# Performance work log

Measured on AMD Instinct MI355X. Metric: run time of the kernel, lower is better.

Reference implementation:

```python
import jax, jax.numpy as jnp
import numpy as np

M = 4  # mixture size of the AttentionStem value embedding

def unfold_windows(a, kh, kw, Hout, Wout):
    # a: [..., Hp, Wp] -> [..., Hout, Wout, kh, kw] (stride-1 sliding windows, cropped)
    rows = []
    for i in range(kh):
        cols = [a[..., i:i + Hout, j:j + Wout] for j in range(kw)]
        rows.append(jnp.stack(cols, axis=-1))
    return jnp.stack(rows, axis=-2)

def attention_stem(x, qw, kw_, vw, emb_a, emb_b, emb_mix, kh, kw, pad):
    # x: [B,Cin,H,W]; qw/kw_: [Cin,Co]; vw: [M,Cin,Co]; emb_a:[Co,kh]; emb_b:[Co,kw]; emb_mix:[M,Co]
    B, Cin, H, W = x.shape
    pl, pr, pt, pb = pad  # F.pad order (left,right,top,bottom)
    xp = jnp.pad(x, ((0, 0), (0, 0), (pt, pb), (pl, pr)))
    Hp, Wp = xp.shape[2], xp.shape[3]
    Hout = min(Hp - kh + 1, H)
    Wout = min(Wp - kw + 1, W)
    q = jnp.einsum('bchw,co->bohw', x[:, :, :Hout, :Wout], qw)       # 1x1 conv query
    k = jnp.einsum('bchw,co->bohw', xp, kw_)                          # 1x1 conv key on padded
    v = jnp.einsum('bchw,mco->mbohw', xp, vw)                         # m 1x1 conv values
    k_win = unfold_windows(k, kh, kw, Hout, Wout)                     # [B,Co,Ho,Wo,kh,kw]
    v_win = unfold_windows(v, kh, kw, Hout, Wout)                     # [M,B,Co,Ho,Wo,kh,kw]
    # mixture relative-position embedding, softmax over mixtures per (kh,kw) offset
    la = emb_mix @ emb_a                                              # [M,kh]
    lb = emb_mix @ emb_b                                              # [M,kw]
    emb = jax.nn.softmax(la[:, :, None] + lb[:, None, :], axis=0)     # [M,kh,kw]
    v_agg = jnp.einsum('mkl,mbohwkl->bohwkl', emb, v_win)             # [B,Co,Ho,Wo,kh,kw]
    K = kh * kw
    scores = jnp.einsum('bohw,bohwkl->bhwkl', q, k_win).reshape(B, Hout, Wout, K)
    attn = jax.nn.softmax(scores, axis=-1).reshape(B, Hout, Wout, kh, kw)
    out = jnp.einsum('bhwkl,bohwkl->bohw', attn, v_agg)               # [B,Co,Ho,Wo]
    return out

def bn_relu(x, g, b):
    # training-mode BatchNorm2d + ReLU
    mu = x.mean(axis=(0, 2, 3), keepdims=True)
    var = x.var(axis=(0, 2, 3), keepdims=True)
    y = (x - mu) * jax.lax.rsqrt(var + 1e-5) * g[None, :, None, None] + b[None, :, None, None]
    return jax.nn.relu(y)

def _params(key):
    ks = jax.random.split(key, 18)
    def w(k, shape):
        return jax.random.normal(k, shape, dtype=jnp.float32) * 0.1
    cfg = [(1, 64, 1, 5), (64, 128, 2, 5), (128, 16, 2, 5)]
    p = {}
    i = 0
    for s, (ci, co, kh, kw) in enumerate(cfg):
        p[f'p{s}_q'] = w(ks[i], (ci, co)); i += 1
        p[f'p{s}_k'] = w(ks[i], (ci, co)); i += 1
        p[f'p{s}_v'] = w(ks[i], (M, ci, co)); i += 1
        p[f'p{s}_ea'] = w(ks[i], (co, kh)); i += 1
        p[f'p{s}_eb'] = w(ks[i], (co, kw)); i += 1
        p[f'p{s}_em'] = w(ks[i], (M, co)); i += 1
        p[f'p{s}_g'] = jnp.ones((co,), jnp.float32)
        p[f'p{s}_b'] = jnp.zeros((co,), jnp.float32)
    return p

def setup_inputs() -> dict:
    key = jax.random.key(0)
    kx, kp = jax.random.split(key)
    inp = {'x': jax.random.normal(kx, (2, 1, 8, 3000), dtype=jnp.float32)}
    inp.update(_params(kp))
    return inp

def reference(x,
              p0_q, p0_k, p0_v, p0_ea, p0_eb, p0_em, p0_g, p0_b,
              p1_q, p1_k, p1_v, p1_ea, p1_eb, p1_em, p1_g, p1_b,
              p2_q, p2_k, p2_v, p2_ea, p2_eb, p2_em, p2_g, p2_b):
    h = attention_stem(x, p0_q, p0_k, p0_v, p0_ea, p0_eb, p0_em, 1, 5, (2, 2, 0, 0))
    h = bn_relu(h, p0_g, p0_b)[:, :, ::2, ::2]                        # MaxPool2d(1,2) == stride-2 subsample
    h = attention_stem(h, p1_q, p1_k, p1_v, p1_ea, p1_eb, p1_em, 2, 5, (2, 2, 1, 1))
    h = bn_relu(h, p1_g, p1_b)[:, :, ::2, ::2]
    h = attention_stem(h, p2_q, p2_k, p2_v, p2_ea, p2_eb, p2_em, 2, 5, (2, 2, 0, 0))
    h = bn_relu(h, p2_g, p2_b)
    B, C, H, W = h.shape
    nW = W // 56                                                       # AvgPool2d((1,56))
    return h[:, :, :, :nW * 56].reshape(B, C, H, nW, 56).mean(-1)
```

## Files before the change

### kernel.cpp

```cpp
#include <hip/hip_runtime.h>
#include <math.h>


#define TPB 256

__global__ void prep0_kernel(const float* __restrict__ ea,
                             const float* __restrict__ eb,
                             const float* __restrict__ em,
                             const float* __restrict__ qw,
                             const float* __restrict__ kw_,
                             const float* __restrict__ vw,
                             float* __restrict__ par) {
    const int M4 = 4, Co = 64, kh = 1, kw = 5;
    __shared__ float la[4];
    __shared__ float lb[20];
    __shared__ float embs[20];
    int tid = threadIdx.x;
    if (tid < 64) {
        float p = qw[tid] * kw_[tid];
#pragma unroll
        for (int d = 1; d < 64; d <<= 1) p += __shfl_xor(p, d, 64);
        if (tid == 0) par[0] = p;
    }
    if (tid >= 64 && tid < 64 + M4) {
        int m = tid - 64;
        float s = 0.f;
        for (int o = 0; o < Co; ++o) s += em[m * Co + o] * ea[o];
        la[m] = s;
    }
    if (tid >= 128 && tid < 128 + M4 * kw) {
        int r = tid - 128;
        int m = r / kw, l = r % kw;
        float s = 0.f;
        for (int o = 0; o < Co; ++o) s += em[m * Co + o] * eb[o * kw + l];
        lb[m * kw + l] = s;
    }
    __syncthreads();
    if (tid < 5) {
        float lg[4];
        float mx = -1e30f;
        for (int m = 0; m < M4; ++m) {
            lg[m] = la[m] + lb[m * kw + tid];
            mx = fmaxf(mx, lg[m]);
        }
        float sum = 0.f;
        for (int m = 0; m < M4; ++m) { lg[m] = expf(lg[m] - mx); sum += lg[m]; }
        float inv = 1.f / sum;
        for (int m = 0; m < M4; ++m) embs[tid * 4 + m] = lg[m] * inv;
    }
    __syncthreads();
    for (int e = tid; e < 5 * 64; e += blockDim.x) {
        int t = e / 64, o = e - t * 64;
        float s = 0.f;
        for (int m = 0; m < M4; ++m) s += embs[t * 4 + m] * vw[m * 64 + o];
        par[1 + e] = s;
    }
}

__global__ void prep_wcat_kernel(const float* __restrict__ ea,
                                 const float* __restrict__ eb,
                                 const float* __restrict__ em,
                                 const float* __restrict__ qw,
                                 const float* __restrict__ kw_,
                                 const float* __restrict__ vw,
                                 float* __restrict__ Wcat,
                                 int Co, int kh, int kw, int Cin) {
    const int M4 = 4;
    __shared__ float la[8];
    __shared__ float lb[20];
    __shared__ float embs[40];
    int K = kh * kw;
    int tid = threadIdx.x;
    if (tid < M4 * kh) {
        int m = tid / kh, k = tid % kh;
        float s = 0.f;
        for (int o = 0; o < Co; ++o) s += em[m * Co + o] * ea[o * kh + k];
        la[tid] = s;
    }
    if (tid >= 64 && tid < 64 + M4 * kw) {
        int r = tid - 64;
        int m = r / kw, l = r % kw;
        float s = 0.f;
        for (int o = 0; o < Co; ++o) s += em[m * Co + o] * eb[o * kw + l];
        lb[r] = s;
    }
    __syncthreads();
    if (tid < K) {
        int k = tid / kw, l = tid % kw;
        float lg[4];
        float mx = -1e30f;
        for (int m = 0; m < M4; ++m) {
            lg[m] = la[m * kh + k] + lb[m * kw + l];
            mx = fmaxf(mx, lg[m]);
        }
        float sum = 0.f;
        for (int m = 0; m < M4; ++m) { lg[m] = expf(lg[m] - mx); sum += lg[m]; }
        float inv = 1.f / sum;
        for (int m = 0; m < M4; ++m) embs[tid * 4 + m] = lg[m] * inv;
    }
    __syncthreads();
    int Mtot = (2 + K) * Co;
    long long total = (long long)Mtot * Cin;
    for (long long e = (long long)blockIdx.x * blockDim.x + tid; e < total;
         e += (long long)gridDim.x * blockDim.x) {
        int m = (int)(e / Cin);
        int c = (int)(e - (long long)m * Cin);
        float val;
        if (m < Co) {
            val = qw[c * Co + m];
        } else if (m < 2 * Co) {
            val = kw_[c * Co + (m - Co)];
        } else {
            int mz = m - 2 * Co;
            int t = mz / Co;
            int o = mz - t * Co;
            val = 0.f;
            for (int mm = 0; mm < M4; ++mm)
                val += embs[t * 4 + mm] * vw[(mm * Cin + c) * Co + o];
        }
        Wcat[e] = val;
    }
}

__global__ void attn_out0_kernel(const float* __restrict__ x,
                                 const float* __restrict__ par,
                                 float* __restrict__ s0) {
    __shared__ float wsh[5][256];
    __shared__ float vsh[5 * 64];
    int tid = threadIdx.x;
    int b = blockIdx.y;
    int n0 = blockIdx.x * 256;
    int n = n0 + tid;
    for (int i = tid; i < 320; i += 256) vsh[i] = par[1 + i];
    float c0 = par[0];
    if (n < 24000) {
        int h = n / 3000, w = n - h * 3000;
        const float* xr = x + b * 24000 + h * 3000;
        float xc = xr[w];
        float xs[5], s[5];
#pragma unroll
        for (int t = 0; t < 5; ++t) {
            int col = w + t - 2;
            xs[t] = (col >= 0 && col < 3000) ? xr[col] : 0.f;
            s[t] = c0 * xc * xs[t];
        }
        float mx = s[0];
#pragma unroll
        for (int t = 1; t < 5; ++t) mx = fmaxf(mx, s[t]);
        float sum = 0.f;
#pragma unroll
        for (int t = 0; t < 5; ++t) { s[t] = expf(s[t] - mx); sum += s[t]; }
        float inv = 1.f / sum;
#pragma unroll
        for (int t = 0; t < 5; ++t) wsh[t][tid] = s[t] * inv * xs[t];
    } else {
#pragma unroll
        for (int t = 0; t < 5; ++t) wsh[t][tid] = 0.f;
    }
    __syncthreads();
    int jq = tid & 63, og = tid >> 6;
    int nq = n0 + jq * 4;
    if (nq < 24000) {
        float wq[5][4];
#pragma unroll
        for (int t = 0; t < 5; ++t)
#pragma unroll
            for (int j = 0; j < 4; ++j) wq[t][j] = wsh[t][jq * 4 + j];
        int obase = og * 16;
        for (int oi = 0; oi < 16; ++oi) {
            int o = obase + oi;
            float4 v;
            v.x = 0.f; v.y = 0.f; v.z = 0.f; v.w = 0.f;
#pragma unroll
            for (int t = 0; t < 5; ++t) {
                float vo = vsh[t * 64 + o];
                v.x = fmaf(wq[t][0], vo, v.x);
                v.y = fmaf(wq[t][1], vo, v.y);
                v.z = fmaf(wq[t][2], vo, v.z);
                v.w = fmaf(wq[t][3], vo, v.w);
            }
            *(float4*)&s0[((size_t)b * 64 + o) * 24000 + nq] = v;
        }
    }
}

__launch_bounds__(256, 2)
__global__ void gemm_qkz_kernel(const float* __restrict__ A,
                                const float* __restrict__ X,
                                float* __restrict__ qk,
                                float* __restrict__ z,
                                int M, int N, int K, int twoCo) {
    __shared__ float As[64][132];
    __shared__ float Bs[64][132];
    int tid = threadIdx.x;
    int b = blockIdx.z;
    int m0 = blockIdx.y * 128, n0 = blockIdx.x * 128;
    int Mz = M - twoCo;
    float acc[8][8] = {{0.f}};
    int am = tid >> 1, ak = (tid & 1) * 32;
    int bk = tid >> 2, bn = (tid & 3) * 32;
    int tm = tid & 15, tn = tid >> 4;

    for (int k0 = 0; k0 < K; k0 += 64) {
        {
            int mA = m0 + am;
            const float* Ap = A + (size_t)mA * K + k0 + ak;
#pragma unroll
            for (int q = 0; q < 8; ++q) {
                float4 v = (mA < M) ? *(const float4*)(Ap + q * 4)
                                    : make_float4(0.f, 0.f, 0.f, 0.f);
                int kk = ak + q * 4;
                As[kk + 0][am] = v.x;
                As[kk + 1][am] = v.y;
                As[kk + 2][am] = v.z;
                As[kk + 3][am] = v.w;
            }
        }
        {
            const float* Xp = X + (size_t)b * K * N + (size_t)(k0 + bk) * N + n0 + bn;
            if (n0 + 128 <= N) {
#pragma unroll
                for (int q = 0; q < 8; ++q)
                    *(float4*)&Bs[bk][bn + q * 4] = *(const float4*)(Xp + q * 4);
            } else {
#pragma unroll
                for (int q = 0; q < 8; ++q)
#pragma unroll
                    for (int j = 0; j < 4; ++j) {
                        int n = n0 + bn + q * 4 + j;
                        Bs[bk][bn + q * 4 + j] = (n < N) ? Xp[q * 4 + j] : 0.f;
                    }
            }
        }
        __syncthreads();
#pragma unroll 16
        for (int k = 0; k < 64; ++k) {
            float4 a0 = *(const float4*)&As[k][tm * 8];
            float4 a1 = *(const float4*)&As[k][tm * 8 + 4];
            float4 b0 = *(const float4*)&Bs[k][tn * 8];
            float4 b1 = *(const float4*)&Bs[k][tn * 8 + 4];
            float av[8] = {a0.x, a0.y, a0.z, a0.w, a1.x, a1.y, a1.z, a1.w};
            float bv[8] = {b0.x, b0.y, b0.z, b0.w, b1.x, b1.y, b1.z, b1.w};
#pragma unroll
            for (int i = 0; i < 8; ++i)
#pragma unroll
                for (int j = 0; j < 8; ++j)
                    acc[i][j] = fmaf(av[i], bv[j], acc[i][j]);
        }
        __syncthreads();
    }
    bool fullN = (n0 + 128 <= N);
#pragma unroll
    for (int i = 0; i < 8; ++i) {
        int m = m0 + tm * 8 + i;
        if (m >= M) continue;
        if (m < twoCo) {
#pragma unroll
            for (int j = 0; j < 8; ++j) {
                int n = n0 + tn * 8 + j;
                if (n < N) qk[((size_t)b * N + n) * twoCo + m] = acc[i][j];
            }
        } else {
            float* zp = &z[((size_t)b * Mz + (m - twoCo)) * N + n0 + tn * 8];
            if (fullN) {
                *(float4*)zp = make_float4(acc[i][0], acc[i][1], acc[i][2], acc[i][3]);
                *(float4*)(zp + 4) = make_float4(acc[i][4], acc[i][5], acc[i][6], acc[i][7]);
            } else {
#pragma unroll
                for (int j = 0; j < 8; ++j) {
                    int n = n0 + tn * 8 + j;
                    if (n < N) zp[j] = acc[i][j];
                }
            }
        }
    }
}

template <int KH, int KW, int CO, int NPB>
__global__ void attn_v3_kernel(const float* __restrict__ qk,
                               float* __restrict__ attn,
                               int H, int W, int Ho, int Wo, int pt, int pl) {
    const int K = KH * KW;
    __shared__ float ssh[NPB][K];
    int tid = threadIdx.x;
    int b = blockIdx.y;
    int ln = tid / K, t = tid - ln * K;
    int Nout = Ho * Wo;
    int n = blockIdx.x * NPB + ln;
    bool active = (tid < NPB * K) && (n < Nout);
    int HWin = H * W;
    float sv = 0.f;
    int ho = 0, wo = 0;
    if (active) {
        ho = n / Wo; wo = n - ho * Wo;
        int row = ho + t / KW - pt, col = wo + t % KW - pl;
        if (row >= 0 && row < H && col >= 0 && col < W) {
            const float* qp = qk + ((size_t)b * HWin + ho * W + wo) * (2 * CO);
            const float* kp = qk + ((size_t)b * HWin + (size_t)row * W + col) * (2 * CO) + CO;
#pragma unroll
            for (int o = 0; o < CO; o += 4) {
                float4 q4 = *(const float4*)(qp + o);
                float4 k4 = *(const float4*)(kp + o);
                sv += q4.x * k4.x + q4.y * k4.y + q4.z * k4.z + q4.w * k4.w;
            }
        }
        ssh[ln][t] = sv;
    }
    __syncthreads();
    if (active) {
        float mx = ssh[ln][0];
#pragma unroll
        for (int tt = 1; tt < K; ++tt) mx = fmaxf(mx, ssh[ln][tt]);
        float sum = 0.f;
#pragma unroll
        for (int tt = 0; tt < K; ++tt) sum += expf(ssh[ln][tt] - mx);
        float num = expf(sv - mx);
        attn[((size_t)b * K + t) * Nout + n] = num / sum;
    }
}

template <int KH, int KW>
__global__ void combine_kernel(const float* __restrict__ z,
                               const float* __restrict__ attn,
                               float* __restrict__ out,
                               int B, int Co, int Mz,
                               int H, int W, int Ho, int Wo,
                               int pt, int pl) {
    const int K = KH * KW;
    int idx = blockIdx.x * blockDim.x + threadIdx.x;
    int N = B * Co * Ho * Wo;
    if (idx >= N) return;
    int wo = idx % Wo; int r = idx / Wo;
    int ho = r % Ho; r /= Ho;
    int o = r % Co; int b = r / Co;
    int Nin = H * W, Nout = Ho * Wo;
    int nout = ho * Wo + wo;
    float acc = 0.f;
#pragma unroll
    for (int dk = 0; dk < KH; ++dk) {
        int row = ho + dk - pt;
        if (row < 0 || row >= H) continue;
#pragma unroll
        for (int dl = 0; dl < KW; ++dl) {
            int col = wo + dl - pl;
            if (col < 0 || col >= W) continue;
            int t = dk * KW + dl;
            float a = attn[((size_t)b * K + t) * Nout + nout];
            float zv = z[((size_t)b * Mz + t * Co + o) * Nin + row * W + col];
            acc = fmaf(a, zv, acc);
        }
    }
    out[idx] = acc;
}

__global__ void bn_partial_kernel(const float* __restrict__ x,
                                  float2* __restrict__ part,
                                  int B, int C, int HW, int len) {
    int c = blockIdx.x, ch = blockIdx.y, NCH = gridDim.y;
    int tid = threadIdx.x;
    int start = ch * len;
    int end = min(HW, start + len);
    float s = 0.f, s2 = 0.f;
    bool vec = ((HW & 3) == 0) && ((len & 3) == 0);
    for (int b = 0; b < B; ++b) {
        const float* xp = x + ((size_t)b * C + c) * HW;
        if (vec) {
            for (int i = start + tid * 4; i < end; i += TPB * 4) {
                float4 v = *(const float4*)(xp + i);
                s += v.x + v.y + v.z + v.w;
                s2 += v.x * v.x + v.y * v.y + v.z * v.z + v.w * v.w;
            }
        } else {
            for (int i = start + tid; i < end; i += TPB) {
                float v = xp[i];
                s += v; s2 += v * v;
            }
        }
    }
    __shared__ float sh[TPB], sh2[TPB];
    sh[tid] = s; sh2[tid] = s2;
    __syncthreads();
    for (int st = TPB / 2; st > 0; st >>= 1) {
        if (tid < st) { sh[tid] += sh[tid + st]; sh2[tid] += sh2[tid + st]; }
        __syncthreads();
    }
    if (tid == 0) part[c * NCH + ch] = make_float2(sh[0], sh2[0]);
}

__global__ void bn_final_kernel(const float2* __restrict__ part,
                                float* __restrict__ mr,
                                int C, int NCH, int B, int HW) {
    int c = threadIdx.x;
    if (c >= C) return;
    double s = 0.0, s2 = 0.0;
    for (int i = 0; i < NCH; ++i) {
        float2 p = part[c * NCH + i];
        s += p.x; s2 += p.y;
    }
    double N = (double)B * HW;
    double mean = s / N;
    double var = s2 / N - mean * mean;
    mr[c] = (float)mean;
    mr[C + c] = (float)(1.0 / sqrt(var + 1e-5));
}

__global__ void bn_pool_kernel(const float* __restrict__ x,
                               const float* __restrict__ mr,
                               const float* __restrict__ g,
                               const float* __restrict__ bb,
                               float* __restrict__ y,
                               int B, int C, int H, int W, int H2, int W2) {
    int idx = blockIdx.x * blockDim.x + threadIdx.x;
    int N = B * C * H2 * W2;
    if (idx >= N) return;
    int w2 = idx % W2; int r = idx / W2;
    int h2 = r % H2; r /= H2;
    int c = r % C; int b = r / C;
    float v = x[(((long long)b * C + c) * H + 2 * h2) * W + 2 * w2];
    float yn = (v - mr[c]) * mr[C + c] * g[c] + bb[c];
    y[idx] = fmaxf(yn, 0.f);
}

__global__ void bn_avg_final_kernel(const float* __restrict__ x,
                                    const float* __restrict__ mr,
                                    const float* __restrict__ g,
                                    const float* __restrict__ bb,
                                    float* __restrict__ out,
                                    int B, int C, int W, int nW) {
    int idx = blockIdx.x * blockDim.x + threadIdx.x;
    int N = B * C * nW;
    if (idx >= N) return;
    int j = idx % nW; int r = idx / nW;
    int c = r % C; int b = r / C;
    float mean = mr[c], rstd = mr[C + c], gg = g[c], bo = bb[c];
    const float* xb = x + ((long long)b * C + c) * W + j * 56;
    float s = 0.f;
    for (int i = 0; i < 56; ++i) {
        float yn = (xb[i] - mean) * rstd * gg + bo;
        s += fmaxf(yn, 0.f);
    }
    out[idx] = s * (1.f / 56.f);
}

extern "C" void kernel_launch(void* const* d_in, const int* in_sizes, int n_in,
                              void* d_out, int out_size, void* d_ws, size_t ws_size,
                              hipStream_t stream) {
    const float* x   = (const float*)d_in[0];
    const float* qw0 = (const float*)d_in[1];
    const float* kw0 = (const float*)d_in[2];
    const float* vw0 = (const float*)d_in[3];
    const float* ea0 = (const float*)d_in[4];
    const float* eb0 = (const float*)d_in[5];
    const float* em0 = (const float*)d_in[6];
    const float* g0  = (const float*)d_in[7];
    const float* b0  = (const float*)d_in[8];
    const float* qw1 = (const float*)d_in[9];
    const float* kw1 = (const float*)d_in[10];
    const float* vw1 = (const float*)d_in[11];
    const float* ea1 = (const float*)d_in[12];
    const float* eb1 = (const float*)d_in[13];
    const float* em1 = (const float*)d_in[14];
    const float* g1  = (const float*)d_in[15];
    const float* b1  = (const float*)d_in[16];
    const float* qw2 = (const float*)d_in[17];
    const float* kw2 = (const float*)d_in[18];
    const float* vw2 = (const float*)d_in[19];
    const float* ea2 = (const float*)d_in[20];
    const float* eb2 = (const float*)d_in[21];
    const float* em2 = (const float*)d_in[22];
    const float* g2  = (const float*)d_in[23];
    const float* b2  = (const float*)d_in[24];
    float* outp = (float*)d_out;
    (void)ws_size; (void)in_sizes; (void)n_in; (void)out_size;

    float* ws = (float*)d_ws;
    size_t off = 0;
    auto alloc = [&](size_t n) { float* p = ws + off; off += (n + 63) & ~(size_t)63; return p; };

    float* arena = alloc(2 * 1280 * 6000);
    float* s0    = arena;
    float* z1    = arena;

    float* par0   = alloc(321);
    float* part   = alloc(2048);
    float* mr0    = alloc(2 * 64);
    float* h0     = alloc(2 * 64 * 6000);
    float* Wcat1  = alloc(1536 * 64);
    float* qk1    = alloc(2 * 6000 * 256);
    float* attn1  = alloc(2 * 10 * 6000);
    float* s1     = alloc(2 * 128 * 6000);
    float* mr1    = alloc(2 * 128);
    float* h1     = alloc(2 * 128 * 1500);
    float* Wcat2  = alloc(192 * 128);
    float* qk2    = alloc(2 * 1500 * 32);
    float* z2     = alloc(2 * 160 * 1500);
    float* attn2  = alloc(2 * 10 * 750);
    float* s2     = alloc(2 * 16 * 750);
    float* mr2    = alloc(2 * 16);

    auto grid = [](int n) { return (n + TPB - 1) / TPB; };

    prep0_kernel<<<1, TPB, 0, stream>>>(ea0, eb0, em0, qw0, kw0, vw0, par0);
    {
        dim3 g(94, 2);
        attn_out0_kernel<<<g, TPB, 0, stream>>>(x, par0, s0);
    }
    {
        dim3 g(64, 8);
        bn_partial_kernel<<<g, TPB, 0, stream>>>(s0, (float2*)part, 2, 64, 24000, 3000);
    }
    bn_final_kernel<<<1, 64, 0, stream>>>((const float2*)part, mr0, 64, 8, 2, 24000);
    bn_pool_kernel<<<grid(2 * 64 * 6000), TPB, 0, stream>>>(s0, mr0, g0, b0, h0,
        2, 64, 8, 3000, 4, 1500);

    prep_wcat_kernel<<<96, TPB, 0, stream>>>(ea1, eb1, em1, qw1, kw1, vw1, Wcat1,
        128, 2, 5, 64);
    {
        dim3 g((6000 + 127) / 128, 1536 / 128, 2);
        gemm_qkz_kernel<<<g, TPB, 0, stream>>>(Wcat1, h0, qk1, z1, 1536, 6000, 64, 256);
    }
    {
        dim3 g(6000 / 25, 2);
        attn_v3_kernel<2, 5, 128, 25><<<g, TPB, 0, stream>>>(qk1, attn1,
            4, 1500, 4, 1500, 1, 2);
    }
    combine_kernel<2, 5><<<grid(2 * 128 * 6000), TPB, 0, stream>>>(z1, attn1, s1,
        2, 128, 1280, 4, 1500, 4, 1500, 1, 2);
    {
        dim3 g(128, 4);
        bn_partial_kernel<<<g, TPB, 0, stream>>>(s1, (float2*)part, 2, 128, 6000, 1500);
    }
    bn_final_kernel<<<1, 128, 0, stream>>>((const float2*)part, mr1, 128, 4, 2, 6000);
    bn_pool_kernel<<<grid(2 * 128 * 1500), TPB, 0, stream>>>(s1, mr1, g1, b1, h1,
        2, 128, 4, 1500, 2, 750);

    prep_wcat_kernel<<<24, TPB, 0, stream>>>(ea2, eb2, em2, qw2, kw2, vw2, Wcat2,
        16, 2, 5, 128);
    {
        dim3 g((1500 + 127) / 128, (192 + 127) / 128, 2);
        gemm_qkz_kernel<<<g, TPB, 0, stream>>>(Wcat2, h1, qk2, z2, 192, 1500, 128, 32);
    }
    {
        dim3 g(750 / 25, 2);
        attn_v3_kernel<2, 5, 16, 25><<<g, TPB, 0, stream>>>(qk2, attn2,
            2, 750, 1, 750, 0, 2);
    }
    combine_kernel<2, 5><<<grid(2 * 16 * 750), TPB, 0, stream>>>(z2, attn2, s2,
        2, 16, 160, 2, 750, 1, 750, 0, 2);
    {
        dim3 g(16, 4);
        bn_partial_kernel<<<g, TPB, 0, stream>>>(s2, (float2*)part, 2, 16, 750, 188);
    }
    bn_final_kernel<<<1, 16, 0, stream>>>((const float2*)part, mr2, 16, 4, 2, 750);
    bn_avg_final_kernel<<<grid(2 * 16 * 13), TPB, 0, stream>>>(s2, mr2, g2, b2, outp,
        2, 16, 750, 13);
}
```

Baseline: 287.8 us.

## Fuse BatchNorm statistics into producer kernels and retile the QKZ GEMM

BatchNorm partial sums are now computed inside the kernels that produce each stage's output (attn_out0 and a new combine_stats kernel). The final mean/rstd reduction is folded into prep_wcat or bn_avg_final, which removes six separate bn_partial/bn_final launches and one extra pass over each activation tensor. The GEMM tile uses a K-step of 32 with a strided thread-to-output mapping and launch bounds of 4 blocks per CU, aiming for higher occupancy and vectorised qk stores. The cost is some redundant per-thread reductions in the final kernel and more warp shuffles in the first stage.

```diff
diff --git a/kernel.cpp b/kernel.cpp
--- a/kernel.cpp
+++ b/kernel.cpp
@@ -11,7 +11,7 @@
                              const float* __restrict__ kw_,
                              const float* __restrict__ vw,
                              float* __restrict__ par) {
-    const int M4 = 4, Co = 64, kh = 1, kw = 5;
+    const int M4 = 4, Co = 64, kw = 5;
     __shared__ float la[4];
     __shared__ float lb[20];
     __shared__ float embs[20];
@@ -64,13 +64,27 @@
                                  const float* __restrict__ kw_,
                                  const float* __restrict__ vw,
                                  float* __restrict__ Wcat,
-                                 int Co, int kh, int kw, int Cin) {
+                                 int Co, int kh, int kw, int Cin,
+                                 const float2* __restrict__ part,
+                                 float* __restrict__ mr,
+                                 int Cprev, int NCH, int count) {
     const int M4 = 4;
     __shared__ float la[8];
     __shared__ float lb[20];
     __shared__ float embs[40];
     int K = kh * kw;
     int tid = threadIdx.x;
+    if (blockIdx.x == 0 && tid < Cprev) {
+        double s = 0.0, s2 = 0.0;
+        for (int i = 0; i < NCH; ++i) {
+            float2 p = part[(size_t)tid * NCH + i];
+            s += p.x; s2 += p.y;
+        }
+        double mean = s / count;
+        double var = s2 / count - mean * mean;
+        mr[tid] = (float)mean;
+        mr[Cprev + tid] = (float)(1.0 / sqrt(var + 1e-5));
+    }
     if (tid < M4 * kh) {
         int m = tid / kh, k = tid % kh;
         float s = 0.f;
@@ -124,7 +138,8 @@
 
 __global__ void attn_out0_kernel(const float* __restrict__ x,
                                  const float* __restrict__ par,
-                                 float* __restrict__ s0) {
+                                 float* __restrict__ s0,
+                                 float2* __restrict__ part0) {
     __shared__ float wsh[5][256];
     __shared__ float vsh[5 * 64];
     int tid = threadIdx.x;
@@ -160,53 +175,61 @@
     __syncthreads();
     int jq = tid & 63, og = tid >> 6;
     int nq = n0 + jq * 4;
-    if (nq < 24000) {
-        float wq[5][4];
-#pragma unroll
-        for (int t = 0; t < 5; ++t)
-#pragma unroll
-            for (int j = 0; j < 4; ++j) wq[t][j] = wsh[t][jq * 4 + j];
-        int obase = og * 16;
-        for (int oi = 0; oi < 16; ++oi) {
-            int o = obase + oi;
-            float4 v;
-            v.x = 0.f; v.y = 0.f; v.z = 0.f; v.w = 0.f;
-#pragma unroll
-            for (int t = 0; t < 5; ++t) {
-                float vo = vsh[t * 64 + o];
-                v.x = fmaf(wq[t][0], vo, v.x);
-                v.y = fmaf(wq[t][1], vo, v.y);
-                v.z = fmaf(wq[t][2], vo, v.z);
-                v.w = fmaf(wq[t][3], vo, v.w);
-            }
-            *(float4*)&s0[((size_t)b * 64 + o) * 24000 + nq] = v;
-        }
-    }
-}
-
-__launch_bounds__(256, 2)
+    bool st = (nq < 24000);
+    float wq[5][4];
+#pragma unroll
+    for (int t = 0; t < 5; ++t)
+#pragma unroll
+        for (int j = 0; j < 4; ++j) wq[t][j] = wsh[t][jq * 4 + j];
+    int obase = og * 16;
+    int chunk = b * gridDim.x + blockIdx.x;
+    for (int oi = 0; oi < 16; ++oi) {
+        int o = obase + oi;
+        float4 v = make_float4(0.f, 0.f, 0.f, 0.f);
+#pragma unroll
+        for (int t = 0; t < 5; ++t) {
+            float vo = vsh[t * 64 + o];
+            v.x = fmaf(wq[t][0], vo, v.x);
+            v.y = fmaf(wq[t][1], vo, v.y);
+            v.z = fmaf(wq[t][2], vo, v.z);
+            v.w = fmaf(wq[t][3], vo, v.w);
+        }
+        if (st) *(float4*)&s0[((size_t)b * 64 + o) * 24000 + nq] = v;
+        float ls = v.x + v.y + v.z + v.w;
+        float ls2 = v.x * v.x + v.y * v.y + v.z * v.z + v.w * v.w;
+#pragma unroll
+        for (int d = 1; d < 64; d <<= 1) {
+            ls += __shfl_xor(ls, d, 64);
+            ls2 += __shfl_xor(ls2, d, 64);
+        }
+        if ((tid & 63) == 0)
+            part0[(size_t)o * 188 + chunk] = make_float2(ls, ls2);
+    }
+}
+
+__launch_bounds__(256, 4)
 __global__ void gemm_qkz_kernel(const float* __restrict__ A,
                                 const float* __restrict__ X,
                                 float* __restrict__ qk,
                                 float* __restrict__ z,
                                 int M, int N, int K, int twoCo) {
-    __shared__ float As[64][132];
-    __shared__ float Bs[64][132];
+    __shared__ float As[32][132];
+    __shared__ float Bs[32][132];
     int tid = threadIdx.x;
     int b = blockIdx.z;
     int m0 = blockIdx.y * 128, n0 = blockIdx.x * 128;
     int Mz = M - twoCo;
     float acc[8][8] = {{0.f}};
-    int am = tid >> 1, ak = (tid & 1) * 32;
-    int bk = tid >> 2, bn = (tid & 3) * 32;
+    int am = tid >> 1, ak = (tid & 1) * 16;
+    int bk = tid >> 3, bn = (tid & 7) * 16;
     int tm = tid & 15, tn = tid >> 4;
 
-    for (int k0 = 0; k0 < K; k0 += 64) {
+    for (int k0 = 0; k0 < K; k0 += 32) {
         {
             int mA = m0 + am;
             const float* Ap = A + (size_t)mA * K + k0 + ak;
 #pragma unroll
-            for (int q = 0; q < 8; ++q) {
+            for (int q = 0; q < 4; ++q) {
                 float4 v = (mA < M) ? *(const float4*)(Ap + q * 4)
                                     : make_float4(0.f, 0.f, 0.f, 0.f);
                 int kk = ak + q * 4;
@@ -220,25 +243,23 @@
             const float* Xp = X + (size_t)b * K * N + (size_t)(k0 + bk) * N + n0 + bn;
             if (n0 + 128 <= N) {
 #pragma unroll
-                for (int q = 0; q < 8; ++q)
+                for (int q = 0; q < 4; ++q)
                     *(float4*)&Bs[bk][bn + q * 4] = *(const float4*)(Xp + q * 4);
             } else {
 #pragma unroll
-                for (int q = 0; q < 8; ++q)
-#pragma unroll
-                    for (int j = 0; j < 4; ++j) {
-                        int n = n0 + bn + q * 4 + j;
-                        Bs[bk][bn + q * 4 + j] = (n < N) ? Xp[q * 4 + j] : 0.f;
-                    }
+                for (int q = 0; q < 16; ++q) {
+                    int n = n0 + bn + q;
+                    Bs[bk][bn + q] = (n < N) ? Xp[q] : 0.f;
+                }
             }
         }
         __syncthreads();
-#pragma unroll 16
-        for (int k = 0; k < 64; ++k) {
-            float4 a0 = *(const float4*)&As[k][tm * 8];
-            float4 a1 = *(const float4*)&As[k][tm * 8 + 4];
-            float4 b0 = *(const float4*)&Bs[k][tn * 8];
-            float4 b1 = *(const float4*)&Bs[k][tn * 8 + 4];
+#pragma unroll 8
+        for (int k = 0; k < 32; ++k) {
+            float4 a0 = *(const float4*)&As[k][tm * 4];
+            float4 a1 = *(const float4*)&As[k][64 + tm * 4];
+            float4 b0 = *(const float4*)&Bs[k][tn * 4];
+            float4 b1 = *(const float4*)&Bs[k][64 + tn * 4];
             float av[8] = {a0.x, a0.y, a0.z, a0.w, a1.x, a1.y, a1.z, a1.w};
             float bv[8] = {b0.x, b0.y, b0.z, b0.w, b1.x, b1.y, b1.z, b1.w};
 #pragma unroll
@@ -251,25 +272,41 @@
     }
     bool fullN = (n0 + 128 <= N);
 #pragma unroll
-    for (int i = 0; i < 8; ++i) {
-        int m = m0 + tm * 8 + i;
-        if (m >= M) continue;
-        if (m < twoCo) {
-#pragma unroll
-            for (int j = 0; j < 8; ++j) {
-                int n = n0 + tn * 8 + j;
-                if (n < N) qk[((size_t)b * N + n) * twoCo + m] = acc[i][j];
-            }
+    for (int iq = 0; iq < 2; ++iq) {
+        int mb = m0 + iq * 64 + tm * 4;
+        if (mb >= M) continue;
+        if (mb < twoCo) {
+#pragma unroll
+            for (int jq = 0; jq < 2; ++jq)
+#pragma unroll
+                for (int jj = 0; jj < 4; ++jj) {
+                    int n = n0 + jq * 64 + tn * 4 + jj;
+                    if (n < N) {
+                        float4 v = make_float4(acc[iq * 4 + 0][jq * 4 + jj],
+                                               acc[iq * 4 + 1][jq * 4 + jj],
+                                               acc[iq * 4 + 2][jq * 4 + jj],
+                                               acc[iq * 4 + 3][jq * 4 + jj]);
+                        *(float4*)&qk[((size_t)b * N + n) * twoCo + mb] = v;
+                    }
+                }
         } else {
-            float* zp = &z[((size_t)b * Mz + (m - twoCo)) * N + n0 + tn * 8];
-            if (fullN) {
-                *(float4*)zp = make_float4(acc[i][0], acc[i][1], acc[i][2], acc[i][3]);
-                *(float4*)(zp + 4) = make_float4(acc[i][4], acc[i][5], acc[i][6], acc[i][7]);
-            } else {
-#pragma unroll
-                for (int j = 0; j < 8; ++j) {
-                    int n = n0 + tn * 8 + j;
-                    if (n < N) zp[j] = acc[i][j];
+#pragma unroll
+            for (int i = 0; i < 4; ++i) {
+                int row = mb + i - twoCo;
+                float* zp = &z[((size_t)b * Mz + row) * N];
+#pragma unroll
+                for (int jq = 0; jq < 2; ++jq) {
+                    int nb_ = n0 + jq * 64 + tn * 4;
+                    if (fullN) {
+                        *(float4*)&zp[nb_] = make_float4(acc[iq * 4 + i][jq * 4 + 0],
+                                                         acc[iq * 4 + i][jq * 4 + 1],
+                                                         acc[iq * 4 + i][jq * 4 + 2],
+                                                         acc[iq * 4 + i][jq * 4 + 3]);
+                    } else {
+#pragma unroll
+                        for (int jj = 0; jj < 4; ++jj)
+                            if (nb_ + jj < N) zp[nb_ + jj] = acc[iq * 4 + i][jq * 4 + jj];
+                    }
                 }
             }
         }
@@ -290,9 +327,8 @@
     bool active = (tid < NPB * K) && (n < Nout);
     int HWin = H * W;
     float sv = 0.f;
-    int ho = 0, wo = 0;
     if (active) {
-        ho = n / Wo; wo = n - ho * Wo;
+        int ho = n / Wo, wo = n - ho * Wo;
         int row = ho + t / KW - pt, col = wo + t % KW - pl;
         if (row >= 0 && row < H && col >= 0 && col < W) {
             const float* qp = qk + ((size_t)b * HWin + ho * W + wo) * (2 * CO);
@@ -320,88 +356,50 @@
 }
 
 template <int KH, int KW>
-__global__ void combine_kernel(const float* __restrict__ z,
-                               const float* __restrict__ attn,
-                               float* __restrict__ out,
-                               int B, int Co, int Mz,
-                               int H, int W, int Ho, int Wo,
-                               int pt, int pl) {
+__global__ void combine_stats_kernel(const float* __restrict__ z,
+                                     const float* __restrict__ attn,
+                                     float* __restrict__ out,
+                                     float2* __restrict__ part,
+                                     int Co, int Mz,
+                                     int H, int W, int Ho, int Wo,
+                                     int pt, int pl) {
     const int K = KH * KW;
-    int idx = blockIdx.x * blockDim.x + threadIdx.x;
-    int N = B * Co * Ho * Wo;
-    if (idx >= N) return;
-    int wo = idx % Wo; int r = idx / Wo;
-    int ho = r % Ho; r /= Ho;
-    int o = r % Co; int b = r / Co;
-    int Nin = H * W, Nout = Ho * Wo;
-    int nout = ho * Wo + wo;
-    float acc = 0.f;
-#pragma unroll
-    for (int dk = 0; dk < KH; ++dk) {
-        int row = ho + dk - pt;
-        if (row < 0 || row >= H) continue;
-#pragma unroll
-        for (int dl = 0; dl < KW; ++dl) {
-            int col = wo + dl - pl;
-            if (col < 0 || col >= W) continue;
-            int t = dk * KW + dl;
-            float a = attn[((size_t)b * K + t) * Nout + nout];
-            float zv = z[((size_t)b * Mz + t * Co + o) * Nin + row * W + col];
-            acc = fmaf(a, zv, acc);
-        }
-    }
-    out[idx] = acc;
-}
-
-__global__ void bn_partial_kernel(const float* __restrict__ x,
-                                  float2* __restrict__ part,
-                                  int B, int C, int HW, int len) {
-    int c = blockIdx.x, ch = blockIdx.y, NCH = gridDim.y;
     int tid = threadIdx.x;
-    int start = ch * len;
-    int end = min(HW, start + len);
-    float s = 0.f, s2 = 0.f;
-    bool vec = ((HW & 3) == 0) && ((len & 3) == 0);
-    for (int b = 0; b < B; ++b) {
-        const float* xp = x + ((size_t)b * C + c) * HW;
-        if (vec) {
-            for (int i = start + tid * 4; i < end; i += TPB * 4) {
-                float4 v = *(const float4*)(xp + i);
-                s += v.x + v.y + v.z + v.w;
-                s2 += v.x * v.x + v.y * v.y + v.z * v.z + v.w * v.w;
+    int bc = blockIdx.y;
+    int b = bc / Co, o = bc - b * Co;
+    int Nout = Ho * Wo, Nin = H * W;
+    int n = blockIdx.x * blockDim.x + tid;
+    float val = 0.f;
+    if (n < Nout) {
+        int ho = n / Wo, wo = n - ho * Wo;
+#pragma unroll
+        for (int dk = 0; dk < KH; ++dk) {
+            int row = ho + dk - pt;
+            if (row < 0 || row >= H) continue;
+#pragma unroll
+            for (int dl = 0; dl < KW; ++dl) {
+                int col = wo + dl - pl;
+                if (col < 0 || col >= W) continue;
+                int t = dk * KW + dl;
+                float a = attn[((size_t)b * K + t) * Nout + n];
+                float zv = z[((size_t)b * Mz + t * Co + o) * Nin + row * W + col];
+                val = fmaf(a, zv, val);
             }
-        } else {
-            for (int i = start + tid; i < end; i += TPB) {
-                float v = xp[i];
-                s += v; s2 += v * v;
-            }
-        }
+        }
+        out[((size_t)b * Co + o) * Nout + n] = val;
     }
     __shared__ float sh[TPB], sh2[TPB];
-    sh[tid] = s; sh2[tid] = s2;
+    sh[tid] = (n < Nout) ? val : 0.f;
+    sh2[tid] = (n < Nout) ? val * val : 0.f;
     __syncthreads();
     for (int st = TPB / 2; st > 0; st >>= 1) {
         if (tid < st) { sh[tid] += sh[tid + st]; sh2[tid] += sh2[tid + st]; }
         __syncthreads();
     }
-    if (tid == 0) part[c * NCH + ch] = make_float2(sh[0], sh2[0]);
-}
-
-__global__ void bn_final_kernel(const float2* __restrict__ part,
-                                float* __restrict__ mr,
-                                int C, int NCH, int B, int HW) {
-    int c = threadIdx.x;
-    if (c >= C) return;
-    double s = 0.0, s2 = 0.0;
-    for (int i = 0; i < NCH; ++i) {
-        float2 p = part[c * NCH + i];
-        s += p.x; s2 += p.y;
-    }
-    double N = (double)B * HW;
-    double mean = s / N;
-    double var = s2 / N - mean * mean;
-    mr[c] = (float)mean;
-    mr[C + c] = (float)(1.0 / sqrt(var + 1e-5));
+    if (tid == 0) {
+        int chunk = b * gridDim.x + blockIdx.x;
+        part[(size_t)o * (2 * gridDim.x) + chunk] = make_float2(sh[0], sh2[0]);
+    }
 }
 
 __global__ void bn_pool_kernel(const float* __restrict__ x,
@@ -422,24 +420,33 @@
 }
 
 __global__ void bn_avg_final_kernel(const float* __restrict__ x,
-                                    const float* __restrict__ mr,
+                                    const float2* __restrict__ part,
                                     const float* __restrict__ g,
                                     const float* __restrict__ bb,
                                     float* __restrict__ out,
-                                    int B, int C, int W, int nW) {
+                                    int B, int C, int W, int nW, int NCH) {
     int idx = blockIdx.x * blockDim.x + threadIdx.x;
     int N = B * C * nW;
     if (idx >= N) return;
     int j = idx % nW; int r = idx / nW;
     int c = r % C; int b = r / C;
-    float mean = mr[c], rstd = mr[C + c], gg = g[c], bo = bb[c];
+    double s = 0.0, s2 = 0.0;
+    for (int i = 0; i < NCH; ++i) {
+        float2 p = part[(size_t)c * NCH + i];
+        s += p.x; s2 += p.y;
+    }
+    double cnt = (double)B * W;
+    double mean = s / cnt;
+    double var = s2 / cnt - mean * mean;
+    float rstd = (float)(1.0 / sqrt(var + 1e-5));
+    float meanf = (float)mean, gg = g[c], bo = bb[c];
     const float* xb = x + ((long long)b * C + c) * W + j * 56;
-    float s = 0.f;
+    float acc = 0.f;
     for (int i = 0; i < 56; ++i) {
-        float yn = (xb[i] - mean) * rstd * gg + bo;
-        s += fmaxf(yn, 0.f);
-    }
-    out[idx] = s * (1.f / 56.f);
+        float yn = (xb[i] - meanf) * rstd * gg + bo;
+        acc += fmaxf(yn, 0.f);
+    }
+    out[idx] = acc * (1.f / 56.f);
 }
 
 extern "C" void kernel_launch(void* const* d_in, const int* in_sizes, int n_in,
@@ -482,7 +489,9 @@
     float* z1    = arena;
 
     float* par0   = alloc(321);
-    float* part   = alloc(2048);
+    float* part0  = alloc(64 * 188 * 2);
+    float* part1  = alloc(128 * 48 * 2);
+    float* part2  = alloc(16 * 6 * 2);
     float* mr0    = alloc(2 * 64);
     float* h0     = alloc(2 * 64 * 6000);
     float* Wcat1  = alloc(1536 * 64);
@@ -496,25 +505,19 @@
     float* z2     = alloc(2 * 160 * 1500);
     float* attn2  = alloc(2 * 10 * 750);
     float* s2     = alloc(2 * 16 * 750);
-    float* mr2    = alloc(2 * 16);
 
     auto grid = [](int n) { return (n + TPB - 1) / TPB; };
 
     prep0_kernel<<<1, TPB, 0, stream>>>(ea0, eb0, em0, qw0, kw0, vw0, par0);
     {
         dim3 g(94, 2);
-        attn_out0_kernel<<<g, TPB, 0, stream>>>(x, par0, s0);
-    }
-    {
-        dim3 g(64, 8);
-        bn_partial_kernel<<<g, TPB, 0, stream>>>(s0, (float2*)part, 2, 64, 24000, 3000);
-    }
-    bn_final_kernel<<<1, 64, 0, stream>>>((const float2*)part, mr0, 64, 8, 2, 24000);
+        attn_out0_kernel<<<g, TPB, 0, stream>>>(x, par0, s0, (float2*)part0);
+    }
+    prep_wcat_kernel<<<96, TPB, 0, stream>>>(ea1, eb1, em1, qw1, kw1, vw1, Wcat1,
+        128, 2, 5, 64, (const float2*)part0, mr0, 64, 188, 48000);
     bn_pool_kernel<<<grid(2 * 64 * 6000), TPB, 0, stream>>>(s0, mr0, g0, b0, h0,
         2, 64, 8, 3000, 4, 1500);
 
-    prep_wcat_kernel<<<96, TPB, 0, stream>>>(ea1, eb1, em1, qw1, kw1, vw1, Wcat1,
-        128, 2, 5, 64);
     {
         dim3 g((6000 + 127) / 128, 1536 / 128, 2);
         gemm_qkz_kernel<<<g, TPB, 0, stream>>>(Wcat1, h0, qk1, z1, 1536, 6000, 64, 256);
@@ -524,18 +527,16 @@
         attn_v3_kernel<2, 5, 128, 25><<<g, TPB, 0, stream>>>(qk1, attn1,
             4, 1500, 4, 1500, 1, 2);
     }
-    combine_kernel<2, 5><<<grid(2 * 128 * 6000), TPB, 0, stream>>>(z1, attn1, s1,
-        2, 128, 1280, 4, 1500, 4, 1500, 1, 2);
-    {
-        dim3 g(128, 4);
-        bn_partial_kernel<<<g, TPB, 0, stream>>>(s1, (float2*)part, 2, 128, 6000, 1500);
-    }
-    bn_final_kernel<<<1, 128, 0, stream>>>((const float2*)part, mr1, 128, 4, 2, 6000);
+    {
+        dim3 g(24, 2 * 128);
+        combine_stats_kernel<2, 5><<<g, TPB, 0, stream>>>(z1, attn1, s1,
+            (float2*)part1, 128, 1280, 4, 1500, 4, 1500, 1, 2);
+    }
+    prep_wcat_kernel<<<24, TPB, 0, stream>>>(ea2, eb2, em2, qw2, kw2, vw2, Wcat2,
+        16, 2, 5, 128, (const float2*)part1, mr1, 128, 48, 12000);
     bn_pool_kernel<<<grid(2 * 128 * 1500), TPB, 0, stream>>>(s1, mr1, g1, b1, h1,
         2, 128, 4, 1500, 2, 750);
 
-    prep_wcat_kernel<<<24, TPB, 0, stream>>>(ea2, eb2, em2, qw2, kw2, vw2, Wcat2,
-        16, 2, 5, 128);
     {
         dim3 g((1500 + 127) / 128, (192 + 127) / 128, 2);
         gemm_qkz_kernel<<<g, TPB, 0, stream>>>(Wcat2, h1, qk2, z2, 192, 1500, 128, 32);
@@ -545,13 +546,11 @@
         attn_v3_kernel<2, 5, 16, 25><<<g, TPB, 0, stream>>>(qk2, attn2,
             2, 750, 1, 750, 0, 2);
     }
-    combine_kernel<2, 5><<<grid(2 * 16 * 750), TPB, 0, stream>>>(z2, attn2, s2,
-        2, 16, 160, 2, 750, 1, 750, 0, 2);
-    {
-        dim3 g(16, 4);
-        bn_partial_kernel<<<g, TPB, 0, stream>>>(s2, (float2*)part, 2, 16, 750, 188);
-    }
-    bn_final_kernel<<<1, 16, 0, stream>>>((const float2*)part, mr2, 16, 4, 2, 750);
-    bn_avg_final_kernel<<<grid(2 * 16 * 13), TPB, 0, stream>>>(s2, mr2, g2, b2, outp,
-        2, 16, 750, 13);
-}
+    {
+        dim3 g(3, 2 * 16);
+        combine_stats_kernel<2, 5><<<g, TPB, 0, stream>>>(z2, attn2, s2,
+            (float2*)part2, 16, 160, 2, 750, 1, 750, 0, 2);
+    }
+    bn_avg_final_kernel<<<grid(2 * 16 * 13), TPB, 0, stream>>>(s2, (const float2*)part2,
+        g2, b2, outp, 2, 16, 750, 13, 6);
+}
```

Measured after the change: 282.2 us. About the same (-1.9%).
